# Optimization experiments

Measured on AMD Instinct MI355X. Metric: run time of the kernel, lower is better.

## Reference

```python
import jax, jax.numpy as jnp
import numpy as np

# PointCNN layer dims
N, NUM_PTS, P, K, DIMS = 32, 2048, 1024, 16, 3
C_IN, C_OUT = 64, 128
C_HALF = C_OUT // 2            # dense lift of raw features
C_MID = C_OUT // 4             # lifted coord features (C_in != 0)
DM = min(int(np.ceil(C_OUT / C_IN)), 4)   # depth multiplier = 2
C_CAT = C_MID + C_HALF         # 96 channels into X-transform matmul
BN_INV = 1.0 / float(np.sqrt(1.0 + 1e-5))  # inference BN, running mean 0 / var 1


def _dense(x, W, b, g, be):
    # Dense = Linear -> ELU -> BatchNorm (inference affine)
    return g * (jax.nn.elu(x @ W + b) * BN_INV) + be


def setup_inputs() -> dict:
    key = jax.random.key(0)
    ks = jax.random.split(key, 24)
    def rn(k, shape, s=0.1):
        return (jax.random.normal(k, shape) * s).astype(jnp.float32)
    return {
        "rep_pts": jax.random.normal(ks[0], (N, P, DIMS), jnp.float32),
        "pts": jax.random.normal(ks[1], (N, NUM_PTS, DIMS), jnp.float32),
        "fts": jax.random.normal(ks[2], (N, NUM_PTS, C_IN), jnp.float32),
        "pts_idx": jax.random.randint(ks[3], (N, P, K), 0, NUM_PTS, dtype=jnp.int32),
        # PointCNN.dense : C_in -> C_out//2
        "d0_W": rn(ks[4], (C_IN, C_HALF)), "d0_b": rn(ks[5], (C_HALF,)),
        "d0_g": jnp.ones((C_HALF,), jnp.float32), "d0_be": rn(ks[6], (C_HALF,)),
        # XConv.dense1 : dims -> C_mid
        "d1_W": rn(ks[7], (DIMS, C_MID)), "d1_b": rn(ks[8], (C_MID,)),
        "d1_g": jnp.ones((C_MID,), jnp.float32), "d1_be": rn(ks[9], (C_MID,)),
        # XConv.dense2 : C_mid -> C_mid
        "d2_W": rn(ks[10], (C_MID, C_MID)), "d2_b": rn(ks[11], (C_MID,)),
        "d2_g": jnp.ones((C_MID,), jnp.float32), "d2_be": rn(ks[12], (C_MID,)),
        # x_trans: Conv2d(dims -> K*K, kernel (1,K)) then 2 Dense (no BN)
        "xc_W": rn(ks[13], (K * K, DIMS, K)), "xc_b": rn(ks[14], (K * K,)),
        "xd1_W": rn(ks[15], (K * K, K * K)), "xd1_b": rn(ks[16], (K * K,)),
        "xd2_W": rn(ks[17], (K * K, K * K)), "xd2_b": rn(ks[18], (K * K,)),
        # end_conv: depthwise (1,K) conv + pointwise conv + ELU + BN
        "dw_W": rn(ks[19], (C_CAT, DM, K)), "dw_b": rn(ks[20], (C_CAT * DM,)),
        "pw_W": rn(ks[21], (C_CAT * DM, C_OUT)), "pw_b": rn(ks[22], (C_OUT,)),
        "end_g": jnp.ones((C_OUT,), jnp.float32), "end_be": rn(ks[23], (C_OUT,)),
    }


def reference(rep_pts, pts, fts, pts_idx, d0_W, d0_b, d0_g, d0_be,
              d1_W, d1_b, d1_g, d1_be, d2_W, d2_b, d2_g, d2_be,
              xc_W, xc_b, xd1_W, xd1_b, xd2_W, xd2_b,
              dw_W, dw_b, pw_W, pw_b, end_g, end_be):
    # lift raw features: Dense C_in -> C_out//2
    fts_l = _dense(fts, d0_W, d0_b, d0_g, d0_be)          # (N, NUM_PTS, C_half)
    # select_region: per-batch irregular neighbor gather
    gather = jax.vmap(lambda a, i: a[i])
    pts_reg = gather(pts, pts_idx)                        # (N,P,K,dims)
    fts_reg = gather(fts_l, pts_idx)                      # (N,P,K,C_half)
    pts_local = pts_reg - rep_pts[:, :, None, :]          # center on rep point
    # lifting MLP on local coordinates
    h = _dense(pts_local, d1_W, d1_b, d1_g, d1_be)
    h = _dense(h, d2_W, d2_b, d2_g, d2_be)                # (N,P,K,C_mid)
    fts_cat = jnp.concatenate([h, fts_reg], axis=-1)      # (N,P,K,C_cat)
    # learned X-transform: Conv2d(dims->K*K, (1,K)) collapses K -> 1, then 2 Dense
    X = jax.nn.elu(jnp.einsum('npkd,qdk->npq', pts_local, xc_W) + xc_b)
    X = jax.nn.elu(X @ xd1_W + xd1_b)
    X = (X @ xd2_W + xd2_b).reshape(pts.shape[0], P, K, K)
    fts_X = jnp.einsum('npij,npjc->npic', X, fts_cat)     # (N,P,K,C_cat)
    # depthwise (groups=C_cat, kernel (1,K)) -> channel layout c*DM+m
    dw = jnp.einsum('npkc,cmk->npcm', fts_X, dw_W)
    dw = dw.reshape(pts.shape[0], P, C_CAT * DM) + dw_b
    # pointwise conv + ELU + inference BN, squeeze collapsed K axis
    out = jax.nn.elu(dw @ pw_W + pw_b)
    return end_g * (out * BN_INV) + end_be                # (N,P,C_out)
```

## Files before the change

kernel.cpp:

```cpp
#include <hip/hip_runtime.h>
#include <math.h>

#define NBATCH 32
#define NUMPT 2048
#define PP 1024
#define MPB 16
#define BN_INV 0.9999950000374996f

typedef __attribute__((ext_vector_type(8))) short short8;
typedef __attribute__((ext_vector_type(4))) short short4v;
typedef __attribute__((ext_vector_type(2))) short short2v;
typedef __attribute__((ext_vector_type(4))) float f32x4;

#define MFMA(a,b,c) __builtin_amdgcn_mfma_f32_16x16x32_bf16(a,b,c,0,0,0)

#define FTSL_ELEMS 4194304
#define OFF_D0F  0
#define OFF_XCF  4096
#define OFF_X1F  20480
#define OFF_X2F  86016
#define OFF_D2F  151552
#define OFF_PWF  152576
#define TOT_FRAG 177152

#define CATP 1552

static __device__ __forceinline__ float eluf(float x) {
    return x > 0.0f ? x : (__expf(x) - 1.0f);
}
static __device__ __forceinline__ short f2bf(float x) {
    union { float f; unsigned u; } v; v.f = x;
    unsigned r = v.u + 0x7FFFu + ((v.u >> 16) & 1u);
    return (short)(r >> 16);
}

__global__ __launch_bounds__(256) void k_prep(
    const float* __restrict__ d0W, const float* __restrict__ xcW,
    const float* __restrict__ xd1W, const float* __restrict__ xd2W,
    const float* __restrict__ d2W, const float* __restrict__ pwW,
    short* __restrict__ wf)
{
    int gid = blockIdx.x * 256 + threadIdx.x;
    if (gid >= TOT_FRAG) return;
    float val;
    if (gid < OFF_XCF) {
        int e = gid, j = e & 7, lane = (e >> 3) & 63, t = e >> 9;
        int nb = t % 4, kt = t / 4;
        int nn = nb * 16 + (lane & 15), k = kt * 32 + (lane >> 4) * 8 + j;
        val = d0W[k * 64 + nn];
    } else if (gid < OFF_X1F) {
        int e = gid - OFF_XCF, j = e & 7, lane = (e >> 3) & 63, t = e >> 9;
        int nb = t % 16, kt = t / 16;
        int q = nb * 16 + (lane & 15), kk = kt * 32 + (lane >> 4) * 8 + j;
        val = (kk < 48) ? xcW[(q * 3 + (kk >> 4)) * 16 + (kk & 15)] : 0.0f;
    } else if (gid < OFF_X2F) {
        int e = gid - OFF_X1F, j = e & 7, lane = (e >> 3) & 63, t = e >> 9;
        int nb = t % 16, kt = t / 16;
        int nn = nb * 16 + (lane & 15), k = kt * 32 + (lane >> 4) * 8 + j;
        val = xd1W[k * 256 + nn];
    } else if (gid < OFF_D2F) {
        int e = gid - OFF_X2F, j = e & 7, lane = (e >> 3) & 63, t = e >> 9;
        int nb = t % 16, kt = t / 16;
        int nn = nb * 16 + (lane & 15), k = kt * 32 + (lane >> 4) * 8 + j;
        val = xd2W[k * 256 + nn];
    } else if (gid < OFF_PWF) {
        int e = gid - OFF_D2F, j = e & 7, lane = (e >> 3) & 63, t = e >> 9;
        int nb = t % 2;
        int nn = nb * 16 + (lane & 15), k = (lane >> 4) * 8 + j;
        val = d2W[k * 32 + nn];
    } else {
        int e = gid - OFF_PWF, j = e & 7, lane = (e >> 3) & 63, t = e >> 9;
        int nb = t % 8, kt = t / 8;
        int nn = nb * 16 + (lane & 15), k = kt * 32 + (lane >> 4) * 8 + j;
        val = pwW[k * 128 + nn];
    }
    wf[gid] = f2bf(val);
}

__global__ __launch_bounds__(256) void k_dense0m(
    const float* __restrict__ fts, const short* __restrict__ wf,
    const float* __restrict__ b, const float* __restrict__ g,
    const float* __restrict__ be, short* __restrict__ fl)
{
    __shared__ __align__(16) short sB[2 * 4160];
    const int tid = threadIdx.x;
    const long base = (long)blockIdx.x * 128 * 64;

    #pragma unroll
    for (int it = 0; it < 4; ++it) {
        const int gidx = tid + it * 256;
        const int r = gidx >> 3, o = gidx & 7;
        float4 va = *(const float4*)&fts[base + r * 64 + o * 8];
        float4 vb = *(const float4*)&fts[base + r * 64 + o * 8 + 4];
        short8 pk;
        pk[0] = f2bf(va.x); pk[1] = f2bf(va.y); pk[2] = f2bf(va.z); pk[3] = f2bf(va.w);
        pk[4] = f2bf(vb.x); pk[5] = f2bf(vb.y); pk[6] = f2bf(vb.z); pk[7] = f2bf(vb.w);
        *(short8*)&sB[(o >> 2) * 4160 + (r >> 4) * 520 + ((o & 3) * 16 + (r & 15)) * 8] = pk;
    }
    __syncthreads();

    const int wave = tid >> 6, lane = tid & 63;
    const int col = lane & 15, quad = lane >> 4;
    const f32x4 fz = {0.f, 0.f, 0.f, 0.f};
    f32x4 acc[2][4] = {{fz, fz, fz, fz}, {fz, fz, fz, fz}};
    const short8* WA = (const short8*)(wf + OFF_D0F);
    #pragma unroll
    for (int kt = 0; kt < 2; ++kt) {
        short8 af[4];
        #pragma unroll
        for (int mt = 0; mt < 4; ++mt) af[mt] = WA[(kt * 4 + mt) * 64 + lane];
        #pragma unroll
        for (int ni = 0; ni < 2; ++ni) {
            short8 bf_ = *(const short8*)&sB[kt * 4160 + (wave * 2 + ni) * 520 + lane * 8];
            #pragma unroll
            for (int mt = 0; mt < 4; ++mt)
                acc[ni][mt] = MFMA(af[mt], bf_, acc[ni][mt]);
        }
    }
    #pragma unroll
    for (int mt = 0; mt < 4; ++mt) {
        const int c0 = mt * 16 + quad * 4;
        float4 b4 = *(const float4*)&b[c0];
        float4 g4 = *(const float4*)&g[c0];
        float4 e4 = *(const float4*)&be[c0];
        #pragma unroll
        for (int ni = 0; ni < 2; ++ni) {
            long rowg = (long)blockIdx.x * 128 + (wave * 2 + ni) * 16 + col;
            short4v sv;
            sv[0] = f2bf(g4.x * (eluf(acc[ni][mt][0] + b4.x) * BN_INV) + e4.x);
            sv[1] = f2bf(g4.y * (eluf(acc[ni][mt][1] + b4.y) * BN_INV) + e4.y);
            sv[2] = f2bf(g4.z * (eluf(acc[ni][mt][2] + b4.z) * BN_INV) + e4.z);
            sv[3] = f2bf(g4.w * (eluf(acc[ni][mt][3] + b4.w) * BN_INV) + e4.w);
            *(short4v*)&fl[rowg * 64 + c0] = sv;
        }
    }
}

__global__ __launch_bounds__(256) void k_xconv(
    const float* __restrict__ rep_pts, const float* __restrict__ pts,
    const int* __restrict__ pts_idx, const short* __restrict__ fl,
    const short* __restrict__ wf,
    const float* __restrict__ d1W, const float* __restrict__ d1b,
    const float* __restrict__ d1g, const float* __restrict__ d1be,
    const float* __restrict__ d2b, const float* __restrict__ d2g,
    const float* __restrict__ d2be,
    const float* __restrict__ xcb, const float* __restrict__ xd1b,
    const float* __restrict__ xd2b,
    const float* __restrict__ dwW, const float* __restrict__ dwb,
    const float* __restrict__ pwb,
    const float* __restrict__ endg, const float* __restrict__ endbe,
    float* __restrict__ out)
{
    __shared__ __align__(16) short s_catF[MPB * CATP];
    __shared__ __align__(16) short s_big[8448];
    __shared__ __align__(16) short s_X0b[4160];
    __shared__ __align__(16) short s_plF[1024];

    const int tid = threadIdx.x;
    const int wave = tid >> 6, lane = tid & 63;
    const int col = lane & 15, quad = lane >> 4;
    const int n = blockIdx.x >> 6;
    const int pb = (blockIdx.x & 63) * MPB;
    const long prow0 = (long)n * PP + pb;
    short* s_h1F = s_big;
    short* s_X1 = s_big;
    short* s_X2 = s_big + 4160;
    short* s_dwF = s_X0b;
    const f32x4 fz = {0.f, 0.f, 0.f, 0.f};
    const short8 zz = {0, 0, 0, 0, 0, 0, 0, 0};

    for (int i = 768 + tid; i < 1024; i += 256) s_plF[i] = 0;
    const int p0 = tid >> 4, k0 = tid & 15;
    const int idxv = pts_idx[(prow0 + p0) * 16 + k0];
    float x0, x1, x2;
    {
        const float* pp = pts + ((long)n * NUMPT + idxv) * 3;
        const float* rp = rep_pts + (prow0 + p0) * 3;
        x0 = pp[0] - rp[0]; x1 = pp[1] - rp[1]; x2 = pp[2] - rp[2];
        const float v[3] = {x0, x1, x2};
        #pragma unroll
        for (int d = 0; d < 3; ++d) {
            int kk = d * 16 + k0;
            s_plF[((kk >> 5) * 64 + ((kk >> 3) & 3) * 16 + p0) * 8 + (kk & 7)] = f2bf(v[d]);
        }
    }

    short8 gv[8];
    {
        const short8* gp = (const short8*)(fl + ((long)n * NUMPT + idxv) * 64);
        #pragma unroll
        for (int i = 0; i < 8; ++i) gv[i] = gp[i];
    }

    #pragma unroll
    for (int oct = 0; oct < 4; ++oct) {
        short8 v8;
        #pragma unroll
        for (int u = 0; u < 8; ++u) {
            int c = oct * 8 + u;
            float z = d1b[c] + x0 * d1W[c] + x1 * d1W[32 + c] + x2 * d1W[64 + c];
            v8[u] = f2bf(d1g[c] * (eluf(z) * BN_INV) + d1be[c]);
        }
        *(short8*)&s_h1F[(p0 * 66 + oct * 16 + k0) * 8] = v8;
    }

    {
        const int gbase = p0 * CATP + 32 * 16 + k0;
        #pragma unroll
        for (int i = 0; i < 8; ++i) {
            #pragma unroll
            for (int u = 0; u < 8; ++u)
                s_catF[gbase + (i * 8 + u) * 16] = gv[i][u];
        }
    }
    __syncthreads();

    {
        const short8* B = (const short8*)(wf + OFF_D2F);
        short8 b0 = B[lane], b1 = B[64 + lane];
        short8 a[4];
        #pragma unroll
        for (int mt0 = 0; mt0 < 4; ++mt0)
            a[mt0] = *(const short8*)&s_h1F[((wave * 4 + mt0) * 66 + lane) * 8];
        #pragma unroll
        for (int nb = 0; nb < 2; ++nb) {
            int c2 = nb * 16 + col;
            float bb = d2b[c2], gg = d2g[c2], bee = d2be[c2];
            #pragma unroll
            for (int mt0 = 0; mt0 < 4; ++mt0) {
                int mt = wave * 4 + mt0;
                f32x4 acc = MFMA(a[mt0], nb ? b1 : b0, fz);
                short4v sv;
                #pragma unroll
                for (int r = 0; r < 4; ++r)
                    sv[r] = f2bf(gg * (eluf(acc[r] + bb) * BN_INV) + bee);
                *(short4v*)&s_catF[mt * CATP + c2 * 16 + quad * 4] = sv;
            }
        }
    }

    {
        short8 a0 = *(const short8*)&s_plF[lane * 8];
        short8 a1 = *(const short8*)&s_plF[(64 + lane) * 8];
        const short8* B = (const short8*)(wf + OFF_XCF);
        #pragma unroll
        for (int t = 0; t < 4; ++t) {
            int nb = wave * 4 + t;
            f32x4 acc = MFMA(a0, B[nb * 64 + lane], fz);
            acc = MFMA(a1, B[(16 + nb) * 64 + lane], acc);
            int q = nb * 16 + col;
            float bq = xcb[q];
            #pragma unroll
            for (int r = 0; r < 4; ++r) {
                int p = quad * 4 + r;
                s_X0b[(q >> 5) * 520 + (((q >> 3) & 3) * 16 + p) * 8 + (q & 7)]
                    = f2bf(eluf(acc[r] + bq));
            }
        }
    }
    __syncthreads();

    {
        short8 a[8];
        #pragma unroll
        for (int kt = 0; kt < 8; ++kt)
            a[kt] = *(const short8*)&s_X0b[kt * 520 + lane * 8];
        const short8* B = (const short8*)(wf + OFF_X1F);
        #pragma unroll
        for (int t = 0; t < 4; ++t) {
            int nb = wave * 4 + t;
            f32x4 acc = fz;
            #pragma unroll
            for (int kt = 0; kt < 8; ++kt)
                acc = MFMA(a[kt], B[(kt * 16 + nb) * 64 + lane], acc);
            int q = nb * 16 + col;
            float bq = xd1b[q];
            #pragma unroll
            for (int r = 0; r < 4; ++r) {
                int p = quad * 4 + r;
                s_X1[(q >> 5) * 520 + (((q >> 3) & 3) * 16 + p) * 8 + (q & 7)]
                    = f2bf(eluf(acc[r] + bq));
            }
        }
    }
    __syncthreads();

    {
        short8 a[8];
        #pragma unroll
        for (int kt = 0; kt < 8; ++kt)
            a[kt] = *(const short8*)&s_X1[kt * 520 + lane * 8];
        const short8* B = (const short8*)(wf + OFF_X2F);
        #pragma unroll
        for (int t = 0; t < 4; ++t) {
            int nb = wave * 4 + t;
            f32x4 acc = fz;
            #pragma unroll
            for (int kt = 0; kt < 8; ++kt)
                acc = MFMA(a[kt], B[(kt * 16 + nb) * 64 + lane], acc);
            float bq = xd2b[nb * 16 + col];
            #pragma unroll
            for (int r = 0; r < 4; ++r) {
                int p = quad * 4 + r;
                s_X2[p * 264 + ((col >> 3) * 16 + nb) * 8 + (col & 7)] = f2bf(acc[r] + bq);
            }
        }
    }
    __syncthreads();

    {
        float4 wd0[6], wd1[6]; float2 bdw[6];
        #pragma unroll
        for (int nb = 0; nb < 6; ++nb) {
            int c = nb * 16 + col;
            wd0[nb] = *(const float4*)&dwW[(c * 2 + 0) * 16 + quad * 4];
            wd1[nb] = *(const float4*)&dwW[(c * 2 + 1) * 16 + quad * 4];
            bdw[nb] = *(const float2*)&dwb[c * 2];
        }
        #pragma unroll
        for (int pi = 0; pi < 4; ++pi) {
            int p = wave * 4 + pi;
            short8 afr = zz;
            if (lane < 32) afr = *(const short8*)&s_X2[p * 264 + lane * 8];
            #pragma unroll
            for (int nb = 0; nb < 6; ++nb) {
                short8 bfr = zz;
                if (lane < 32)
                    bfr = *(const short8*)&s_catF[p * CATP + (nb * 16 + col) * 16 + quad * 8];
                f32x4 acc = MFMA(afr, bfr, fz);
                float q0 = acc[0] * wd0[nb].x + acc[1] * wd0[nb].y + acc[2] * wd0[nb].z + acc[3] * wd0[nb].w;
                float q1 = acc[0] * wd1[nb].x + acc[1] * wd1[nb].y + acc[2] * wd1[nb].z + acc[3] * wd1[nb].w;
                q0 += __shfl_xor(q0, 16); q0 += __shfl_xor(q0, 32);
                q1 += __shfl_xor(q1, 16); q1 += __shfl_xor(q1, 32);
                if (quad == 0) {
                    int c2 = col * 2;
                    int ad = (nb * 64 + (c2 >> 3) * 16 + p) * 8 + (c2 & 7);
                    short2v sv2;
                    sv2[0] = f2bf(q0 + bdw[nb].x);
                    sv2[1] = f2bf(q1 + bdw[nb].y);
                    *(short2v*)&s_dwF[ad] = sv2;
                }
            }
        }
    }
    __syncthreads();

    {
        short8 a[6];
        #pragma unroll
        for (int kt = 0; kt < 6; ++kt)
            a[kt] = *(const short8*)&s_dwF[(kt * 64 + lane) * 8];
        const short8* B = (const short8*)(wf + OFF_PWF);
        #pragma unroll
        for (int t = 0; t < 2; ++t) {
            int nb = wave * 2 + t;
            f32x4 acc = fz;
            #pragma unroll
            for (int kt = 0; kt < 6; ++kt)
                acc = MFMA(a[kt], B[(kt * 8 + nb) * 64 + lane], acc);
            int o = nb * 16 + col;
            float bo = pwb[o], go = endg[o], beo = endbe[o];
            #pragma unroll
            for (int r = 0; r < 4; ++r) {
                int p = quad * 4 + r;
                out[(prow0 + p) * 128 + o] = go * (eluf(acc[r] + bo) * BN_INV) + beo;
            }
        }
    }
}

extern "C" void kernel_launch(void* const* d_in, const int* in_sizes, int n_in,
                              void* d_out, int out_size, void* d_ws, size_t ws_size,
                              hipStream_t stream) {
    const float* rep_pts = (const float*)d_in[0];
    const float* pts     = (const float*)d_in[1];
    const float* fts     = (const float*)d_in[2];
    const int*   pts_idx = (const int*)d_in[3];
    const float* d0W = (const float*)d_in[4];
    const float* d0b = (const float*)d_in[5];
    const float* d0g = (const float*)d_in[6];
    const float* d0be = (const float*)d_in[7];
    const float* d1W = (const float*)d_in[8];
    const float* d1b = (const float*)d_in[9];
    const float* d1g = (const float*)d_in[10];
    const float* d1be = (const float*)d_in[11];
    const float* d2W = (const float*)d_in[12];
    const float* d2b = (const float*)d_in[13];
    const float* d2g = (const float*)d_in[14];
    const float* d2be = (const float*)d_in[15];
    const float* xcW = (const float*)d_in[16];
    const float* xcb = (const float*)d_in[17];
    const float* xd1W = (const float*)d_in[18];
    const float* xd1b = (const float*)d_in[19];
    const float* xd2W = (const float*)d_in[20];
    const float* xd2b = (const float*)d_in[21];
    const float* dwW = (const float*)d_in[22];
    const float* dwb = (const float*)d_in[23];
    const float* pwW = (const float*)d_in[24];
    const float* pwb = (const float*)d_in[25];
    const float* endg = (const float*)d_in[26];
    const float* endbe = (const float*)d_in[27];
    float* out = (float*)d_out;

    short* wsS = (short*)d_ws;
    short* fl = wsS;
    short* wf = wsS + FTSL_ELEMS;

    k_prep<<<(TOT_FRAG + 255) / 256, 256, 0, stream>>>(d0W, xcW, xd1W, xd2W, d2W, pwW, wf);
    k_dense0m<<<(NBATCH * NUMPT) / 128, 256, 0, stream>>>(fts, wf, d0b, d0g, d0be, fl);
    k_xconv<<<NBATCH * (PP / MPB), 256, 0, stream>>>(
        rep_pts, pts, pts_idx, fl, wf,
        d1W, d1b, d1g, d1be, d2b, d2g, d2be,
        xcb, xd1b, xd2b, dwW, dwb, pwb, endg, endbe, out);
}
```

Measured before the change: 197.9 us.

## Fuse dense0 feature lift into the xconv gather kernel

Removes the separate dense0 kernel and its bf16 intermediate buffer. The xconv kernel now gathers raw fp32 neighbour features, converts them to bf16, and applies the 64→64 dense+ELU+BN with MFMA in shared memory before the X-transform. This saves a launch and the intermediate write/read round trip. In exchange, the dense is recomputed for every neighbour (K times redundant), the gather reads twice the bytes, and extra block syncs are added.

After: 217.6 us. +10.0%, slower.

```diff
diff --git a/kernel.cpp b/kernel.cpp
--- a/kernel.cpp
+++ b/kernel.cpp
@@ -14,7 +14,6 @@
 
 #define MFMA(a,b,c) __builtin_amdgcn_mfma_f32_16x16x32_bf16(a,b,c,0,0,0)
 
-#define FTSL_ELEMS 4194304
 #define OFF_D0F  0
 #define OFF_XCF  4096
 #define OFF_X1F  20480
@@ -77,69 +76,12 @@
     wf[gid] = f2bf(val);
 }
 
-__global__ __launch_bounds__(256) void k_dense0m(
-    const float* __restrict__ fts, const short* __restrict__ wf,
-    const float* __restrict__ b, const float* __restrict__ g,
-    const float* __restrict__ be, short* __restrict__ fl)
-{
-    __shared__ __align__(16) short sB[2 * 4160];
-    const int tid = threadIdx.x;
-    const long base = (long)blockIdx.x * 128 * 64;
-
-    #pragma unroll
-    for (int it = 0; it < 4; ++it) {
-        const int gidx = tid + it * 256;
-        const int r = gidx >> 3, o = gidx & 7;
-        float4 va = *(const float4*)&fts[base + r * 64 + o * 8];
-        float4 vb = *(const float4*)&fts[base + r * 64 + o * 8 + 4];
-        short8 pk;
-        pk[0] = f2bf(va.x); pk[1] = f2bf(va.y); pk[2] = f2bf(va.z); pk[3] = f2bf(va.w);
-        pk[4] = f2bf(vb.x); pk[5] = f2bf(vb.y); pk[6] = f2bf(vb.z); pk[7] = f2bf(vb.w);
-        *(short8*)&sB[(o >> 2) * 4160 + (r >> 4) * 520 + ((o & 3) * 16 + (r & 15)) * 8] = pk;
-    }
-    __syncthreads();
-
-    const int wave = tid >> 6, lane = tid & 63;
-    const int col = lane & 15, quad = lane >> 4;
-    const f32x4 fz = {0.f, 0.f, 0.f, 0.f};
-    f32x4 acc[2][4] = {{fz, fz, fz, fz}, {fz, fz, fz, fz}};
-    const short8* WA = (const short8*)(wf + OFF_D0F);
-    #pragma unroll
-    for (int kt = 0; kt < 2; ++kt) {
-        short8 af[4];
-        #pragma unroll
-        for (int mt = 0; mt < 4; ++mt) af[mt] = WA[(kt * 4 + mt) * 64 + lane];
-        #pragma unroll
-        for (int ni = 0; ni < 2; ++ni) {
-            short8 bf_ = *(const short8*)&sB[kt * 4160 + (wave * 2 + ni) * 520 + lane * 8];
-            #pragma unroll
-            for (int mt = 0; mt < 4; ++mt)
-                acc[ni][mt] = MFMA(af[mt], bf_, acc[ni][mt]);
-        }
-    }
-    #pragma unroll
-    for (int mt = 0; mt < 4; ++mt) {
-        const int c0 = mt * 16 + quad * 4;
-        float4 b4 = *(const float4*)&b[c0];
-        float4 g4 = *(const float4*)&g[c0];
-        float4 e4 = *(const float4*)&be[c0];
-        #pragma unroll
-        for (int ni = 0; ni < 2; ++ni) {
-            long rowg = (long)blockIdx.x * 128 + (wave * 2 + ni) * 16 + col;
-            short4v sv;
-            sv[0] = f2bf(g4.x * (eluf(acc[ni][mt][0] + b4.x) * BN_INV) + e4.x);
-            sv[1] = f2bf(g4.y * (eluf(acc[ni][mt][1] + b4.y) * BN_INV) + e4.y);
-            sv[2] = f2bf(g4.z * (eluf(acc[ni][mt][2] + b4.z) * BN_INV) + e4.z);
-            sv[3] = f2bf(g4.w * (eluf(acc[ni][mt][3] + b4.w) * BN_INV) + e4.w);
-            *(short4v*)&fl[rowg * 64 + c0] = sv;
-        }
-    }
-}
-
 __global__ __launch_bounds__(256) void k_xconv(
     const float* __restrict__ rep_pts, const float* __restrict__ pts,
-    const int* __restrict__ pts_idx, const short* __restrict__ fl,
+    const int* __restrict__ pts_idx, const float* __restrict__ fts,
     const short* __restrict__ wf,
+    const float* __restrict__ d0b, const float* __restrict__ d0g,
+    const float* __restrict__ d0be,
     const float* __restrict__ d1W, const float* __restrict__ d1b,
     const float* __restrict__ d1g, const float* __restrict__ d1be,
     const float* __restrict__ d2b, const float* __restrict__ d2g,
@@ -162,6 +104,7 @@
     const int n = blockIdx.x >> 6;
     const int pb = (blockIdx.x & 63) * MPB;
     const long prow0 = (long)n * PP + pb;
+    short* s_stage = s_big;
     short* s_h1F = s_big;
     short* s_X1 = s_big;
     short* s_X2 = s_big + 4160;
@@ -185,11 +128,56 @@
         }
     }
 
-    short8 gv[8];
-    {
-        const short8* gp = (const short8*)(fl + ((long)n * NUMPT + idxv) * 64);
-        #pragma unroll
-        for (int i = 0; i < 8; ++i) gv[i] = gp[i];
+    short8 ar[8];
+    {
+        const float4* rowp = (const float4*)(fts + ((long)n * NUMPT + idxv) * 64);
+        #pragma unroll
+        for (int h = 0; h < 8; ++h) {
+            float4 va = rowp[2 * h], vb = rowp[2 * h + 1];
+            short8 pk;
+            pk[0] = f2bf(va.x); pk[1] = f2bf(va.y); pk[2] = f2bf(va.z); pk[3] = f2bf(va.w);
+            pk[4] = f2bf(vb.x); pk[5] = f2bf(vb.y); pk[6] = f2bf(vb.z); pk[7] = f2bf(vb.w);
+            ar[h] = pk;
+        }
+    }
+
+    float b0r[4], g0r[4], be0r[4];
+    #pragma unroll
+    for (int nb = 0; nb < 4; ++nb) {
+        int c = nb * 16 + col;
+        b0r[nb] = d0b[c]; g0r[nb] = d0g[c]; be0r[nb] = d0be[c];
+    }
+
+    const short8* B0 = (const short8*)(wf + OFF_D0F);
+    #pragma unroll
+    for (int P = 0; P < 2; ++P) {
+        if ((p0 >> 3) == P) {
+            const int mtp = p0 & 7;
+            #pragma unroll
+            for (int kt = 0; kt < 2; ++kt)
+                #pragma unroll
+                for (int o = 0; o < 4; ++o)
+                    *(short8*)&s_stage[(mtp * 2 + kt) * 520 + (k0 + 16 * o) * 8] = ar[kt * 4 + o];
+        }
+        __syncthreads();
+        #pragma unroll
+        for (int i = 0; i < 2; ++i) {
+            const int mtp = wave * 2 + i;
+            short8 a0 = *(const short8*)&s_stage[(mtp * 2 + 0) * 520 + lane * 8];
+            short8 a1 = *(const short8*)&s_stage[(mtp * 2 + 1) * 520 + lane * 8];
+            const int p = P * 8 + mtp;
+            #pragma unroll
+            for (int nb = 0; nb < 4; ++nb) {
+                f32x4 acc = MFMA(a0, B0[nb * 64 + lane], fz);
+                acc = MFMA(a1, B0[(4 + nb) * 64 + lane], acc);
+                short4v sv;
+                #pragma unroll
+                for (int r = 0; r < 4; ++r)
+                    sv[r] = f2bf(g0r[nb] * (eluf(acc[r] + b0r[nb]) * BN_INV) + be0r[nb]);
+                *(short4v*)&s_catF[p * CATP + (32 + nb * 16 + col) * 16 + quad * 4] = sv;
+            }
+        }
+        __syncthreads();
     }
 
     #pragma unroll
@@ -202,16 +190,6 @@
             v8[u] = f2bf(d1g[c] * (eluf(z) * BN_INV) + d1be[c]);
         }
         *(short8*)&s_h1F[(p0 * 66 + oct * 16 + k0) * 8] = v8;
-    }
-
-    {
-        const int gbase = p0 * CATP + 32 * 16 + k0;
-        #pragma unroll
-        for (int i = 0; i < 8; ++i) {
-            #pragma unroll
-            for (int u = 0; u < 8; ++u)
-                s_catF[gbase + (i * 8 + u) * 16] = gv[i][u];
-        }
     }
     __syncthreads();
 
@@ -402,14 +380,12 @@
     const float* endbe = (const float*)d_in[27];
     float* out = (float*)d_out;
 
-    short* wsS = (short*)d_ws;
-    short* fl = wsS;
-    short* wf = wsS + FTSL_ELEMS;
+    short* wf = (short*)d_ws;
 
     k_prep<<<(TOT_FRAG + 255) / 256, 256, 0, stream>>>(d0W, xcW, xd1W, xd2W, d2W, pwW, wf);
-    k_dense0m<<<(NBATCH * NUMPT) / 128, 256, 0, stream>>>(fts, wf, d0b, d0g, d0be, fl);
     k_xconv<<<NBATCH * (PP / MPB), 256, 0, stream>>>(
-        rep_pts, pts, pts_idx, fl, wf,
+        rep_pts, pts, pts_idx, fts, wf,
+        d0b, d0g, d0be,
         d1W, d1b, d1g, d1be, d2b, d2g, d2be,
         xcb, xd1b, xd2b, dwW, dwb, pwb, endg, endbe, out);
 }
```
